# Kernel tuning notes

Measured on AMD Instinct MI355X. Metric: run time of the kernel, lower is better.

Reference implementation:

```python
import jax, jax.numpy as jnp
import numpy as np

B, S, ENC, DEC, ATTN, H = 256, 512, 256, 256, 128, 48

def setup_inputs() -> dict:
    key = jax.random.key(0)
    ks = jax.random.split(key, 12)
    n = jax.random.normal
    return {
        'enc_outputs': n(ks[0], (B, S, ENC), jnp.float32),
        'h0': n(ks[1], (B, DEC), jnp.float32),
        'c0': n(ks[2], (B, DEC), jnp.float32),
        'W_enc': n(ks[3], (ENC, ATTN), jnp.float32) * 0.05,
        'W_dec': n(ks[4], (DEC, ATTN), jnp.float32) * 0.05,
        'v': n(ks[5], (ATTN,), jnp.float32) * 0.05,
        'W_ih': n(ks[6], (4 * DEC, 1 + ENC), jnp.float32) * 0.05,
        'W_hh': n(ks[7], (4 * DEC, DEC), jnp.float32) * 0.05,
        'b_ih': n(ks[8], (4 * DEC,), jnp.float32) * 0.05,
        'b_hh': n(ks[9], (4 * DEC,), jnp.float32) * 0.05,
        'W_out': n(ks[10], (DEC,), jnp.float32) * 0.05,
        'b_out': n(ks[11], (1,), jnp.float32) * 0.05,
    }

def reference(enc_outputs, h0, c0, W_enc, W_dec, v, W_ih, W_hh, b_ih, b_hh, W_out, b_out):
    # Precompute encoder projection (constant across timesteps; same math as per-step).
    enc_proj = jnp.einsum('bse,ea->bsa', enc_outputs, W_enc)  # [B,S,ATTN]
    batch = enc_outputs.shape[0]
    inp0 = jnp.zeros((batch, 1), enc_outputs.dtype)

    def step(carry, _):
        h, c, inp = carry
        dec_proj = h @ W_dec  # [B,ATTN]
        scores = jnp.tanh(enc_proj + dec_proj[:, None, :]) @ v  # [B,S]
        attn_w = jax.nn.softmax(scores, axis=-1)
        context = jnp.einsum('bs,bse->be', attn_w, enc_outputs)  # [B,ENC]
        rnn_in = jnp.concatenate([inp, context], axis=-1)  # [B,1+ENC]
        gates = rnn_in @ W_ih.T + b_ih + h @ W_hh.T + b_hh  # [B,4*DEC]
        i, f, g, o = jnp.split(gates, 4, axis=-1)  # PyTorch LSTMCell gate order
        c_new = jax.nn.sigmoid(f) * c + jax.nn.sigmoid(i) * jnp.tanh(g)
        h_new = jax.nn.sigmoid(o) * jnp.tanh(c_new)
        out = h_new @ W_out + b_out[0]  # [B]
        return (h_new, c_new, out[:, None]), (out, attn_w)

    _, (preds, attn_seq) = jax.lax.scan(step, (h0, c0, inp0), None, length=H)
    preds = jnp.transpose(preds, (1, 0))        # [B,H]
    attn_seq = jnp.transpose(attn_seq, (1, 0, 2))  # [B,H,S]
    return preds, attn_seq
```

## Files before the change

kernel.cpp:

```cpp
#include <hip/hip_runtime.h>
#include <stdint.h>

#define LOG2E 1.4426950408889634f
#define SCOPE __HIP_MEMORY_SCOPE_AGENT

typedef short v8s __attribute__((ext_vector_type(8)));
typedef float v4f __attribute__((ext_vector_type(4)));

__device__ __forceinline__ uint32_t bf16r(float x){
  uint32_t u = __float_as_uint(x);
  return (u + 0x7fffu + ((u >> 16) & 1u)) >> 16;
}
__device__ __forceinline__ uint32_t pack2(float lo, float hi){
  return bf16r(lo) | (bf16r(hi) << 16);
}
__device__ __forceinline__ float unlo(uint32_t u){ return __uint_as_float(u << 16); }
__device__ __forceinline__ float unhi(uint32_t u){ return __uint_as_float(u & 0xffff0000u); }

__device__ __forceinline__ float fexp2(float x){ return __builtin_amdgcn_exp2f(x); }
__device__ __forceinline__ float frcp(float x){ return __builtin_amdgcn_rcpf(x); }
__device__ __forceinline__ float ftanh(float x){
  float e = fexp2(x * (2.0f * LOG2E));
  return 1.0f - 2.0f * frcp(e + 1.0f);
}
__device__ __forceinline__ float fsig(float x){
  return frcp(1.0f + fexp2(-x * LOG2E));
}
__device__ __forceinline__ float wave_sum(float x){
  #pragma unroll
  for(int o = 32; o; o >>= 1) x += __shfl_xor(x, o, 64);
  return x;
}

__device__ __forceinline__ unsigned flag_ld(const unsigned* p){
  return __hip_atomic_load(p, __ATOMIC_RELAXED, SCOPE);
}
__device__ __forceinline__ void flag_st(unsigned* p, unsigned v){
  __hip_atomic_store(p, v, __ATOMIC_RELAXED, SCOPE);
}
__device__ __forceinline__ float ldf_c(const float* p){
  return __hip_atomic_load(p, __ATOMIC_RELAXED, SCOPE);
}
__device__ __forceinline__ void stf_c(float* p, float v){
  __hip_atomic_store(p, v, __ATOMIC_RELAXED, SCOPE);
}
__device__ __forceinline__ uint64_t ld64_c(const uint64_t* p){
  return __hip_atomic_load(p, __ATOMIC_RELAXED, SCOPE);
}
__device__ __forceinline__ void st64_c(uint64_t* p, uint64_t v){
  __hip_atomic_store(p, v, __ATOMIC_RELAXED, SCOPE);
}
__device__ __forceinline__ void st16_c(unsigned short* p, unsigned short v){
  __hip_atomic_store(p, v, __ATOMIC_RELAXED, SCOPE);
}

__device__ __forceinline__ int gate_row(int jg){
  return (jg & 3) * 256 + (jg >> 6) * 16 + ((jg >> 2) & 15);
}

__global__ __launch_bounds__(256) void k_pack(const float* __restrict__ W_ih,
                                              const float* __restrict__ W_hh,
                                              const float* __restrict__ b_ih,
                                              const float* __restrict__ b_hh,
                                              const float* __restrict__ W_enc,
                                              unsigned short* __restrict__ WmT,
                                              float* __restrict__ biasc,
                                              float* __restrict__ w0v,
                                              unsigned short* __restrict__ WencTh,
                                              unsigned short* __restrict__ WencTl){
  int gid = blockIdx.x * 256 + threadIdx.x;
  if(gid < 65536){
    int jg = gid >> 6, k8 = gid & 63;
    int row = gate_row(jg);
    int k0 = k8 * 8;
    uint32_t p[4];
    #pragma unroll
    for(int mm = 0; mm < 4; ++mm){
      int ka = k0 + 2 * mm, kb = ka + 1;
      float lo = (ka < 256) ? W_ih[row * 257 + 1 + ka] : W_hh[row * 256 + (ka - 256)];
      float hi = (kb < 256) ? W_ih[row * 257 + 1 + kb] : W_hh[row * 256 + (kb - 256)];
      p[mm] = pack2(lo, hi);
    }
    *(uint4*)&WmT[(size_t)jg * 512 + k0] = make_uint4(p[0], p[1], p[2], p[3]);
    if(k8 == 0){
      biasc[jg] = b_ih[row] + b_hh[row];
      w0v[jg] = W_ih[row * 257];
    }
  } else {
    int g2 = gid - 65536;
    int k = g2 >> 7, a = g2 & 127;
    float x = W_enc[k * 128 + a];
    uint32_t hb = bf16r(x);
    WencTh[a * 256 + k] = (unsigned short)hb;
    float hv = __uint_as_float(hb << 16);
    WencTl[a * 256 + k] = (unsigned short)bf16r(x - hv);
  }
}

__global__ __launch_bounds__(256, 2) void k_enc_proj(const float* __restrict__ enc,
                                                     const unsigned short* __restrict__ WencTh,
                                                     const unsigned short* __restrict__ WencTl,
                                                     unsigned short* __restrict__ ep,
                                                     unsigned short* __restrict__ encbT){
  __shared__ unsigned short Ash[128][48];
  __shared__ unsigned short Asl[128][48];
  __shared__ unsigned short Wth[128][48];
  __shared__ unsigned short Wtl[128][48];
  const int tid = threadIdx.x;
  const int b = blockIdx.x >> 2, mt = blockIdx.x & 3;
  const int lane = tid & 63, w = tid >> 6;
  const int rr = lane & 15, quad = lane >> 4;

  v4f acc[2][8];
  #pragma unroll
  for(int g = 0; g < 2; ++g)
    #pragma unroll
    for(int nt = 0; nt < 8; ++nt) acc[g][nt] = (v4f){0.f, 0.f, 0.f, 0.f};

  const float* encBase = enc + ((size_t)(b * 512 + mt * 128)) * 256;

  for(int kt = 0; kt < 8; ++kt){
    __syncthreads();
    #pragma unroll
    for(int i = 0; i < 4; ++i){
      int flat = i * 256 + tid;
      int row = flat >> 3, c4 = flat & 7;
      float4 f = *(const float4*)(encBase + (size_t)row * 256 + kt * 32 + c4 * 4);
      uint32_t hx = bf16r(f.x), hy = bf16r(f.y), hz = bf16r(f.z), hw = bf16r(f.w);
      uint2 hp = make_uint2(hx | (hy << 16), hz | (hw << 16));
      float lx = f.x - __uint_as_float(hx << 16);
      float ly = f.y - __uint_as_float(hy << 16);
      float lz = f.z - __uint_as_float(hz << 16);
      float lw = f.w - __uint_as_float(hw << 16);
      uint2 lp = make_uint2(pack2(lx, ly), pack2(lz, lw));
      *(uint2*)&Ash[row][c4 * 4] = hp;
      *(uint2*)&Asl[row][c4 * 4] = lp;
    }
    #pragma unroll
    for(int i = 0; i < 2; ++i){
      int flat = i * 256 + tid;
      int a = flat >> 2, q4 = flat & 3;
      *(uint4*)&Wth[a][q4 * 8] = *(const uint4*)(WencTh + (size_t)a * 256 + kt * 32 + q4 * 8);
      *(uint4*)&Wtl[a][q4 * 8] = *(const uint4*)(WencTl + (size_t)a * 256 + kt * 32 + q4 * 8);
    }
    __syncthreads();
    #pragma unroll
    for(int g = 0; g < 2; ++g){
      v8s ah = *(const v8s*)&Ash[32 * w + 16 * g + rr][quad * 8];
      v8s al = *(const v8s*)&Asl[32 * w + 16 * g + rr][quad * 8];
      #pragma unroll
      for(int nt = 0; nt < 8; ++nt){
        v8s bh = *(const v8s*)&Wth[nt * 16 + rr][quad * 8];
        v8s bl = *(const v8s*)&Wtl[nt * 16 + rr][quad * 8];
        acc[g][nt] = __builtin_amdgcn_mfma_f32_16x16x32_bf16(ah, bh, acc[g][nt], 0, 0, 0);
        acc[g][nt] = __builtin_amdgcn_mfma_f32_16x16x32_bf16(al, bh, acc[g][nt], 0, 0, 0);
        acc[g][nt] = __builtin_amdgcn_mfma_f32_16x16x32_bf16(ah, bl, acc[g][nt], 0, 0, 0);
      }
    }
    {
      unsigned short* ebT = encbT + ((size_t)(b * 256 + kt * 32)) * 512 + mt * 128;
      #pragma unroll
      for(int i2 = 0; i2 < 2; ++i2){
        int flat = i2 * 256 + tid;
        int e_loc = flat & 31, sc = flat >> 5;
        unsigned short tmp[8];
        #pragma unroll
        for(int i = 0; i < 8; ++i) tmp[i] = Ash[sc * 8 + i][e_loc];
        *(uint4*)&ebT[(size_t)e_loc * 512 + sc * 8] = *(uint4*)tmp;
      }
    }
  }
  #pragma unroll
  for(int g = 0; g < 2; ++g){
    int s0 = 128 * mt + 32 * w + 16 * g + quad * 4;
    #pragma unroll
    for(int nt = 0; nt < 8; ++nt){
      int a = nt * 16 + rr;
      uint2 pp = make_uint2(pack2(acc[g][nt][0], acc[g][nt][1]),
                            pack2(acc[g][nt][2], acc[g][nt][3]));
      *(uint2*)&ep[((size_t)b * 128 + a) * 512 + s0] = pp;
    }
  }
}

__global__ __launch_bounds__(512) void k_zero(unsigned* __restrict__ fl){
  fl[threadIdx.x] = 0u;
}

__global__ __launch_bounds__(512, 2) void k_steps(
    const unsigned short* __restrict__ encbT, const unsigned short* __restrict__ ep,
    const unsigned short* __restrict__ WmT, const float* __restrict__ biasc,
    const float* __restrict__ w0v, const float* __restrict__ Wdec,
    const float* __restrict__ Wout, const float* __restrict__ h0,
    const float* __restrict__ c0, const float* __restrict__ v,
    const float* __restrict__ b_out, unsigned* __restrict__ flagA,
    unsigned* __restrict__ flagB, float* __restrict__ predf,
    float* __restrict__ dpp, float* __restrict__ predp,
    unsigned short* __restrict__ xcat2, float* __restrict__ out)
{
  __shared__ __align__(16) unsigned short WT[64][520];
  __shared__ __align__(16) unsigned short AT[16][520];
  __shared__ float WdecL[16][128];
  __shared__ float gact[64][20];
  __shared__ float dpf[128];
  __shared__ float vl[128];
  __shared__ float scp[64][65];
  __shared__ float red2[8];
  __shared__ float hf[256];
  __shared__ float dppart[4][128];
  __shared__ __align__(16) unsigned short abfh[512];
  __shared__ __align__(16) unsigned short abfl[512];
  __shared__ float biasL[64], w0L[64], WoutL[16], predfL[16];
  __shared__ float sB;

  const int tid = threadIdx.x, b = blockIdx.x;
  const int lane = tid & 63, wid = tid >> 6;
  const int quad = lane >> 4, rr = lane & 15;
  const int m16 = (b >> 4) << 4;
  const int n = b & 15;

  {
    const uint4* src = (const uint4*)(WmT + (size_t)(n * 64) * 512);
    #pragma unroll
    for(int i = 0; i < 8; ++i){
      int flat = i * 512 + tid;
      int r = flat >> 6, q = flat & 63;
      *(uint4*)&WT[r][q * 8] = src[r * 64 + q];
    }
    const float4* wsrc = (const float4*)(Wdec + (size_t)(n * 16) * 128);
    int r2 = tid >> 5, q2 = tid & 31;
    *(float4*)&WdecL[r2][q2 * 4] = wsrc[r2 * 32 + q2];
    if(tid < 64){ biasL[tid] = biasc[n * 64 + tid]; w0L[tid] = w0v[n * 64 + tid]; }
    if(tid < 16) WoutL[tid] = Wout[n * 16 + tid];
    if(tid < 128) vl[tid] = v[tid];
    if(tid == 0){ sB = b_out[0]; stf_c(&predf[b], 0.f); }
    #pragma unroll
    for(int i = 0; i < 8; ++i){
      int flat = i * 512 + tid;
      int r = flat >> 8, c = flat & 255;
      AT[r][256 + c] = (unsigned short)bf16r(h0[(size_t)(m16 + r) * 256 + c]);
    }
  }
  float c_reg = 0.f;
  if(tid < 256){
    int bl = tid >> 4, dl = tid & 15;
    c_reg = c0[(size_t)(m16 + bl) * 256 + n * 16 + dl];
    hf[tid] = h0[(size_t)b * 256 + tid];
  }
  __syncthreads();
  {
    int a = tid & 127, p = tid >> 7;
    float s = 0.f;
    const float* wd = Wdec + (size_t)(p * 64) * 128 + a;
    #pragma unroll 8
    for(int d = 0; d < 64; ++d) s += hf[p * 64 + d] * wd[(size_t)d * 128];
    dppart[p][a] = s;
  }
  __syncthreads();
  if(tid < 128) dpf[tid] = dppart[0][tid] + dppart[1][tid] + dppart[2][tid] + dppart[3][tid];
  __syncthreads();

  const uint4* ep4 = (const uint4*)(ep + (size_t)b * 65536);

  #pragma unroll 1
  for(int t = 0; t < 48; ++t){
    unsigned short* xcatP = xcat2 + (size_t)(t & 1) * 131072;
    unsigned short* xcatN = xcat2 + (size_t)((t + 1) & 1) * 131072;

    if(t > 0){
      if(tid < 16){
        unsigned want = (unsigned)t;
        while(flag_ld(&flagB[m16 + tid]) < want) __builtin_amdgcn_s_sleep(1);
      }
      __syncthreads();
      {
        const uint64_t* hsrc = (const uint64_t*)(xcatP + (size_t)m16 * 512);
        #pragma unroll
        for(int i = 0; i < 2; ++i){
          int flat = i * 512 + tid;
          int r = flat >> 6, q = flat & 63;
          *(uint64_t*)&AT[r][256 + q * 4] = ld64_c(hsrc + (size_t)r * 128 + 64 + q);
        }
      }
      if(tid < 128){
        float s = 0.f;
        #pragma unroll
        for(int nn = 0; nn < 16; ++nn) s += ldf_c(&dpp[((size_t)b * 16 + nn) * 128 + tid]);
        dpf[tid] = s;
      } else if(tid == 128){
        float pf = 0.f;
        #pragma unroll
        for(int nn = 0; nn < 16; ++nn) pf += ldf_c(&predp[nn * 256 + b]);
        pf += sB;
        out[b * 48 + (t - 1)] = pf;
        stf_c(&predf[b], pf);
      }
      __syncthreads();
    }

    uint4 u[16];
    #pragma unroll
    for(int i = 0; i < 16; ++i) u[i] = ep4[(wid * 16 + i) * 64 + lane];

    v4f acc = {0.f, 0.f, 0.f, 0.f};
    if(tid < 256){
      const int jl = (tid >> 6) * 16 + rr;
      #pragma unroll
      for(int kt = 8; kt < 16; ++kt){
        int k0 = kt * 32 + quad * 8;
        v8s av = *(const v8s*)&AT[rr][k0];
        v8s bv = *(const v8s*)&WT[jl][k0];
        acc = __builtin_amdgcn_mfma_f32_16x16x32_bf16(av, bv, acc, 0, 0, 0);
      }
    }

    {
      float sc[8];
      #pragma unroll
      for(int j = 0; j < 8; ++j) sc[j] = 0.f;
      #pragma unroll
      for(int i = 0; i < 16; ++i){
        int a = wid * 16 + i;
        float dd = dpf[a], vv = vl[a];
        sc[0] += vv * ftanh(unlo(u[i].x) + dd);
        sc[1] += vv * ftanh(unhi(u[i].x) + dd);
        sc[2] += vv * ftanh(unlo(u[i].y) + dd);
        sc[3] += vv * ftanh(unhi(u[i].y) + dd);
        sc[4] += vv * ftanh(unlo(u[i].z) + dd);
        sc[5] += vv * ftanh(unhi(u[i].z) + dd);
        sc[6] += vv * ftanh(unlo(u[i].w) + dd);
        sc[7] += vv * ftanh(unhi(u[i].w) + dd);
      }
      #pragma unroll
      for(int j = 0; j < 8; ++j) scp[j * 8 + wid][lane] = sc[j];
    }
    __syncthreads();

    float wexp;
    {
      float s = 0.f;
      #pragma unroll
      for(int q = 0; q < 8; ++q) s += scp[(tid & 7) * 8 + q][tid >> 3];
      wexp = fexp2(s * LOG2E);
      float sw = wave_sum(wexp);
      if(lane == 0) red2[wid] = sw;
    }
    __syncthreads();
    {
      float L = red2[0];
      #pragma unroll
      for(int i = 1; i < 8; ++i) L += red2[i];
      float aw = wexp * frcp(L);
      uint32_t ah = bf16r(aw);
      abfh[tid] = (unsigned short)ah;
      abfl[tid] = (unsigned short)bf16r(aw - __uint_as_float(ah << 16));
      out[12288 + (size_t)b * 24576 + t * 512 + tid] = aw;
    }
    __syncthreads();

    {
      const unsigned short* eT =
          encbT + ((size_t)(b * 256) + wid * 32 + rr) * 512 + quad * 8;
      v4f ca = {0.f, 0.f, 0.f, 0.f}, cb = {0.f, 0.f, 0.f, 0.f};
      #pragma unroll 4
      for(int kt = 0; kt < 16; ++kt){
        int k0 = kt * 32;
        v8s avh = *(const v8s*)&abfh[k0 + quad * 8];
        v8s avl = *(const v8s*)&abfl[k0 + quad * 8];
        v8s bv0 = *(const v8s*)(eT + k0);
        v8s bv1 = *(const v8s*)(eT + 16 * 512 + k0);
        ca = __builtin_amdgcn_mfma_f32_16x16x32_bf16(avh, bv0, ca, 0, 0, 0);
        ca = __builtin_amdgcn_mfma_f32_16x16x32_bf16(avl, bv0, ca, 0, 0, 0);
        cb = __builtin_amdgcn_mfma_f32_16x16x32_bf16(avh, bv1, cb, 0, 0, 0);
        cb = __builtin_amdgcn_mfma_f32_16x16x32_bf16(avl, bv1, cb, 0, 0, 0);
      }
      if(quad == 0){
        st16_c(&xcatP[(size_t)b * 512 + wid * 32 + rr], (unsigned short)bf16r(ca[0]));
        st16_c(&xcatP[(size_t)b * 512 + wid * 32 + 16 + rr], (unsigned short)bf16r(cb[0]));
      }
    }
    __syncthreads();
    if(tid == 0) flag_st(&flagA[b], (unsigned)(t + 1));

    if(tid < 16){
      unsigned want = (unsigned)(t + 1);
      while(flag_ld(&flagA[m16 + tid]) < want) __builtin_amdgcn_s_sleep(1);
    }
    __syncthreads();
    {
      const uint64_t* csrc = (const uint64_t*)(xcatP + (size_t)m16 * 512);
      #pragma unroll
      for(int i = 0; i < 2; ++i){
        int flat = i * 512 + tid;
        int r = flat >> 6, q = flat & 63;
        *(uint64_t*)&AT[r][q * 4] = ld64_c(csrc + (size_t)r * 128 + q);
      }
      if(tid < 16) predfL[tid] = ldf_c(&predf[m16 + tid]);
    }
    __syncthreads();
    if(tid < 256){
      const int jl = (tid >> 6) * 16 + rr;
      #pragma unroll
      for(int kt = 0; kt < 8; ++kt){
        int k0 = kt * 32 + quad * 8;
        v8s av = *(const v8s*)&AT[rr][k0];
        v8s bv = *(const v8s*)&WT[jl][k0];
        acc = __builtin_amdgcn_mfma_f32_16x16x32_bf16(av, bv, acc, 0, 0, 0);
      }
      float bias = biasL[jl], w0 = w0L[jl];
      int gate = jl & 3;
      #pragma unroll
      for(int r = 0; r < 4; ++r){
        int bl = quad * 4 + r;
        float pre = acc[r] + bias + predfL[bl] * w0;
        gact[jl][bl] = (gate == 2) ? ftanh(pre) : fsig(pre);
      }
    }
    __syncthreads();
    if(tid < 256){
      int bl = tid >> 4, dl = tid & 15;
      float gi = gact[dl * 4 + 0][bl];
      float gf = gact[dl * 4 + 1][bl];
      float gg = gact[dl * 4 + 2][bl];
      float go = gact[dl * 4 + 3][bl];
      int bg = m16 + bl, dg = n * 16 + dl;
      float cn = gf * c_reg + gi * gg;
      c_reg = cn;
      float hn = go * ftanh(cn);
      st16_c(&xcatN[(size_t)bg * 512 + 256 + dg], (unsigned short)bf16r(hn));
      float pp = hn * WoutL[dl];
      #pragma unroll
      for(int o = 8; o; o >>= 1) pp += __shfl_xor(pp, o, 64);
      if(dl == 0) stf_c(&predp[n * 256 + bg], pp);
      float a0[8] = {0, 0, 0, 0, 0, 0, 0, 0};
      #pragma unroll
      for(int d = 0; d < 16; ++d){
        float hv = __shfl(hn, (lane & 48) + d, 64);
        #pragma unroll
        for(int j = 0; j < 8; ++j) a0[j] += hv * WdecL[d][dl * 8 + j];
      }
      float* dst = &dpp[((size_t)bg * 16 + n) * 128 + dl * 8];
      #pragma unroll
      for(int j = 0; j < 4; ++j){
        uint64_t uu = (uint64_t)__float_as_uint(a0[2 * j]) |
                      ((uint64_t)__float_as_uint(a0[2 * j + 1]) << 32);
        st64_c((uint64_t*)(dst + 2 * j), uu);
      }
    }
    __syncthreads();
    if(tid == 0) flag_st(&flagB[b], (unsigned)(t + 1));
  }

  if(tid < 16){
    while(flag_ld(&flagB[m16 + tid]) < 48u) __builtin_amdgcn_s_sleep(1);
  }
  __syncthreads();
  if(tid == 0){
    float pf = 0.f;
    #pragma unroll
    for(int nn = 0; nn < 16; ++nn) pf += ldf_c(&predp[nn * 256 + b]);
    out[b * 48 + 47] = pf + sB;
  }
}

extern "C" void kernel_launch(void* const* d_in, const int* in_sizes, int n_in,
                              void* d_out, int out_size, void* d_ws, size_t ws_size,
                              hipStream_t stream) {
  (void)in_sizes; (void)n_in; (void)out_size; (void)ws_size;
  const float* enc  = (const float*)d_in[0];
  const float* h0   = (const float*)d_in[1];
  const float* c0   = (const float*)d_in[2];
  const float* Wenc = (const float*)d_in[3];
  const float* Wdec = (const float*)d_in[4];
  const float* v    = (const float*)d_in[5];
  const float* Wih  = (const float*)d_in[6];
  const float* Whh  = (const float*)d_in[7];
  const float* bih  = (const float*)d_in[8];
  const float* bhh  = (const float*)d_in[9];
  const float* Wout = (const float*)d_in[10];
  const float* bout = (const float*)d_in[11];
  float* out = (float*)d_out;
  uint8_t* p = (uint8_t*)d_ws;

  unsigned short* encbT = (unsigned short*)p; p += 67108864ull;
  unsigned short* ep = (unsigned short*)p;  p += 33554432ull;
  unsigned short* WmT = (unsigned short*)p; p += 1048576ull;
  float* biasc  = (float*)p;                p += 4096ull;
  float* w0v    = (float*)p;                p += 4096ull;
  unsigned short* WencTh = (unsigned short*)p; p += 131072ull;
  unsigned short* WencTl = (unsigned short*)p; p += 131072ull;
  float* dpp    = (float*)p;                p += 2097152ull;
  float* predp  = (float*)p;                p += 16384ull;
  unsigned short* xcat2 = (unsigned short*)p; p += 524288ull;

  unsigned* flagA = (unsigned*)WencTh;
  unsigned* flagB = flagA + 256;
  float*    predf = (float*)(flagA + 512);

  k_pack<<<dim3(384), dim3(256), 0, stream>>>(Wih, Whh, bih, bhh, Wenc, WmT, biasc, w0v,
                                              WencTh, WencTl);
  k_enc_proj<<<dim3(1024), dim3(256), 0, stream>>>(enc, WencTh, WencTl, ep, encbT);
  k_zero<<<dim3(1), dim3(512), 0, stream>>>(flagA);
  k_steps<<<dim3(256), dim3(512), 0, stream>>>(encbT, ep, WmT, biasc, w0v, Wdec, Wout,
                                               h0, c0, v, bout, flagA, flagB, predf,
                                               dpp, predp, xcat2, out);
}
```

Measured before the change: 1.241 ms.

## Double step-kernel block size, restructure score loop and dec projection via MFMA

The persistent step kernel now runs 1024 threads per block instead of 512. The attention-score loop is reorganised so each thread handles one sequence position over half of the attention dimension, reading the encoder projection directly rather than staging it in registers. The per-step h@W_dec partial product moves from a scalar FMA loop to bf16 MFMA with a hi/lo split of h and W_dec. The context MFMA is split across more waves, the context is staged in LDS before a coalesced store, and predp is transposed for contiguous reads. The extra threads are meant to raise latency hiding and parallelism, at the cost of more registers and LDS pressure per block and some extra barriers.

```diff
diff --git a/kernel.cpp b/kernel.cpp
--- a/kernel.cpp
+++ b/kernel.cpp
@@ -187,7 +187,7 @@
   fl[threadIdx.x] = 0u;
 }
 
-__global__ __launch_bounds__(512, 2) void k_steps(
+__global__ __launch_bounds__(1024, 4) void k_steps(
     const unsigned short* __restrict__ encbT, const unsigned short* __restrict__ ep,
     const unsigned short* __restrict__ WmT, const float* __restrict__ biasc,
     const float* __restrict__ w0v, const float* __restrict__ Wdec,
@@ -195,21 +195,24 @@
     const float* __restrict__ c0, const float* __restrict__ v,
     const float* __restrict__ b_out, unsigned* __restrict__ flagA,
     unsigned* __restrict__ flagB, float* __restrict__ predf,
-    float* __restrict__ dpp, float* __restrict__ predp,
+    float* __restrict__ dpp, float* __restrict__ predpT,
     unsigned short* __restrict__ xcat2, float* __restrict__ out)
 {
   __shared__ __align__(16) unsigned short WT[64][520];
   __shared__ __align__(16) unsigned short AT[16][520];
-  __shared__ float WdecL[16][128];
+  __shared__ __align__(16) unsigned short WbB1[8][4][16][8];
+  __shared__ __align__(16) unsigned short WbB2[8][4][16][8];
+  __shared__ __align__(16) unsigned short hbfA[16 * 40];
   __shared__ float gact[64][20];
   __shared__ float dpf[128];
   __shared__ float vl[128];
-  __shared__ float scp[64][65];
+  __shared__ float scpS[2][512];
   __shared__ float red2[8];
   __shared__ float hf[256];
   __shared__ float dppart[4][128];
   __shared__ __align__(16) unsigned short abfh[512];
   __shared__ __align__(16) unsigned short abfl[512];
+  __shared__ __align__(16) unsigned short ctxb[256];
   __shared__ float biasL[64], w0L[64], WoutL[16], predfL[16];
   __shared__ float sB;
 
@@ -222,21 +225,32 @@
   {
     const uint4* src = (const uint4*)(WmT + (size_t)(n * 64) * 512);
     #pragma unroll
-    for(int i = 0; i < 8; ++i){
-      int flat = i * 512 + tid;
+    for(int i = 0; i < 4; ++i){
+      int flat = i * 1024 + tid;
       int r = flat >> 6, q = flat & 63;
       *(uint4*)&WT[r][q * 8] = src[r * 64 + q];
     }
-    const float4* wsrc = (const float4*)(Wdec + (size_t)(n * 16) * 128);
-    int r2 = tid >> 5, q2 = tid & 31;
-    *(float4*)&WdecL[r2][q2 * 4] = wsrc[r2 * 32 + q2];
+    #pragma unroll
+    for(int i = 0; i < 2; ++i){
+      int flat = i * 1024 + tid;
+      int d = flat >> 7, a = flat & 127;
+      float wv = Wdec[(size_t)(n * 16 + d) * 128 + a];
+      uint32_t hb = bf16r(wv);
+      float hv = __uint_as_float(hb << 16);
+      uint32_t lb = bf16r(wv - hv);
+      int ac = a >> 4, cr = a & 15, qd = d >> 3, ii = d & 7;
+      WbB1[ac][qd][cr][ii] = (unsigned short)hb;
+      WbB1[ac][2 + qd][cr][ii] = (unsigned short)hb;
+      WbB2[ac][qd][cr][ii] = (unsigned short)lb;
+      WbB2[ac][2 + qd][cr][ii] = 0;
+    }
     if(tid < 64){ biasL[tid] = biasc[n * 64 + tid]; w0L[tid] = w0v[n * 64 + tid]; }
     if(tid < 16) WoutL[tid] = Wout[n * 16 + tid];
     if(tid < 128) vl[tid] = v[tid];
     if(tid == 0){ sB = b_out[0]; stf_c(&predf[b], 0.f); }
     #pragma unroll
-    for(int i = 0; i < 8; ++i){
-      int flat = i * 512 + tid;
+    for(int i = 0; i < 4; ++i){
+      int flat = i * 1024 + tid;
       int r = flat >> 8, c = flat & 255;
       AT[r][256 + c] = (unsigned short)bf16r(h0[(size_t)(m16 + r) * 256 + c]);
     }
@@ -248,7 +262,7 @@
     hf[tid] = h0[(size_t)b * 256 + tid];
   }
   __syncthreads();
-  {
+  if(tid < 512){
     int a = tid & 127, p = tid >> 7;
     float s = 0.f;
     const float* wd = Wdec + (size_t)(p * 64) * 128 + a;
@@ -260,8 +274,6 @@
   if(tid < 128) dpf[tid] = dppart[0][tid] + dppart[1][tid] + dppart[2][tid] + dppart[3][tid];
   __syncthreads();
 
-  const uint4* ep4 = (const uint4*)(ep + (size_t)b * 65536);
-
   #pragma unroll 1
   for(int t = 0; t < 48; ++t){
     unsigned short* xcatP = xcat2 + (size_t)(t & 1) * 131072;
@@ -275,12 +287,8 @@
       __syncthreads();
       {
         const uint64_t* hsrc = (const uint64_t*)(xcatP + (size_t)m16 * 512);
-        #pragma unroll
-        for(int i = 0; i < 2; ++i){
-          int flat = i * 512 + tid;
-          int r = flat >> 6, q = flat & 63;
-          *(uint64_t*)&AT[r][256 + q * 4] = ld64_c(hsrc + (size_t)r * 128 + 64 + q);
-        }
+        int r = tid >> 6, q = tid & 63;
+        *(uint64_t*)&AT[r][256 + q * 4] = ld64_c(hsrc + (size_t)r * 128 + 64 + q);
       }
       if(tid < 128){
         float s = 0.f;
@@ -290,17 +298,13 @@
       } else if(tid == 128){
         float pf = 0.f;
         #pragma unroll
-        for(int nn = 0; nn < 16; ++nn) pf += ldf_c(&predp[nn * 256 + b]);
+        for(int nn = 0; nn < 16; ++nn) pf += ldf_c(&predpT[b * 16 + nn]);
         pf += sB;
         out[b * 48 + (t - 1)] = pf;
         stf_c(&predf[b], pf);
       }
       __syncthreads();
     }
-
-    uint4 u[16];
-    #pragma unroll
-    for(int i = 0; i < 16; ++i) u[i] = ep4[(wid * 16 + i) * 64 + lane];
 
     v4f acc = {0.f, 0.f, 0.f, 0.f};
     if(tid < 256){
@@ -315,72 +319,62 @@
     }
 
     {
-      float sc[8];
-      #pragma unroll
-      for(int j = 0; j < 8; ++j) sc[j] = 0.f;
-      #pragma unroll
-      for(int i = 0; i < 16; ++i){
-        int a = wid * 16 + i;
-        float dd = dpf[a], vv = vl[a];
-        sc[0] += vv * ftanh(unlo(u[i].x) + dd);
-        sc[1] += vv * ftanh(unhi(u[i].x) + dd);
-        sc[2] += vv * ftanh(unlo(u[i].y) + dd);
-        sc[3] += vv * ftanh(unhi(u[i].y) + dd);
-        sc[4] += vv * ftanh(unlo(u[i].z) + dd);
-        sc[5] += vv * ftanh(unhi(u[i].z) + dd);
-        sc[6] += vv * ftanh(unlo(u[i].w) + dd);
-        sc[7] += vv * ftanh(unhi(u[i].w) + dd);
-      }
-      #pragma unroll
-      for(int j = 0; j < 8; ++j) scp[j * 8 + wid][lane] = sc[j];
-    }
-    __syncthreads();
-
-    float wexp;
+      int s = tid & 511, ah = tid >> 9;
+      const unsigned short* eps = ep + (size_t)b * 65536 + (size_t)(ah * 64) * 512 + s;
+      float sc = 0.f;
+      #pragma unroll 8
+      for(int a = 0; a < 64; ++a){
+        float ev = __uint_as_float((uint32_t)eps[(size_t)a * 512] << 16);
+        int ag = ah * 64 + a;
+        sc += vl[ag] * ftanh(ev + dpf[ag]);
+      }
+      scpS[ah][s] = sc;
+    }
+    __syncthreads();
+
+    float aw = 0.f;
     {
-      float s = 0.f;
-      #pragma unroll
-      for(int q = 0; q < 8; ++q) s += scp[(tid & 7) * 8 + q][tid >> 3];
-      wexp = fexp2(s * LOG2E);
-      float sw = wave_sum(wexp);
-      if(lane == 0) red2[wid] = sw;
-    }
-    __syncthreads();
-    {
-      float L = red2[0];
-      #pragma unroll
-      for(int i = 1; i < 8; ++i) L += red2[i];
-      float aw = wexp * frcp(L);
-      uint32_t ah = bf16r(aw);
-      abfh[tid] = (unsigned short)ah;
-      abfl[tid] = (unsigned short)bf16r(aw - __uint_as_float(ah << 16));
-      out[12288 + (size_t)b * 24576 + t * 512 + tid] = aw;
+      float wexp = 0.f;
+      if(tid < 512){
+        float s = scpS[0][tid] + scpS[1][tid];
+        wexp = fexp2(s * LOG2E);
+        float sw = wave_sum(wexp);
+        if(lane == 0) red2[wid] = sw;
+      }
+      __syncthreads();
+      if(tid < 512){
+        float L = red2[0];
+        #pragma unroll
+        for(int i = 1; i < 8; ++i) L += red2[i];
+        aw = wexp * frcp(L);
+        uint32_t ah2 = bf16r(aw);
+        abfh[tid] = (unsigned short)ah2;
+        abfl[tid] = (unsigned short)bf16r(aw - __uint_as_float(ah2 << 16));
+      }
     }
     __syncthreads();
 
     {
       const unsigned short* eT =
-          encbT + ((size_t)(b * 256) + wid * 32 + rr) * 512 + quad * 8;
-      v4f ca = {0.f, 0.f, 0.f, 0.f}, cb = {0.f, 0.f, 0.f, 0.f};
-      #pragma unroll 4
+          encbT + ((size_t)(b * 256) + wid * 16 + rr) * 512 + quad * 8;
+      v4f ca = {0.f, 0.f, 0.f, 0.f};
+      #pragma unroll 8
       for(int kt = 0; kt < 16; ++kt){
         int k0 = kt * 32;
         v8s avh = *(const v8s*)&abfh[k0 + quad * 8];
         v8s avl = *(const v8s*)&abfl[k0 + quad * 8];
-        v8s bv0 = *(const v8s*)(eT + k0);
-        v8s bv1 = *(const v8s*)(eT + 16 * 512 + k0);
-        ca = __builtin_amdgcn_mfma_f32_16x16x32_bf16(avh, bv0, ca, 0, 0, 0);
-        ca = __builtin_amdgcn_mfma_f32_16x16x32_bf16(avl, bv0, ca, 0, 0, 0);
-        cb = __builtin_amdgcn_mfma_f32_16x16x32_bf16(avh, bv1, cb, 0, 0, 0);
-        cb = __builtin_amdgcn_mfma_f32_16x16x32_bf16(avl, bv1, cb, 0, 0, 0);
-      }
-      if(quad == 0){
-        st16_c(&xcatP[(size_t)b * 512 + wid * 32 + rr], (unsigned short)bf16r(ca[0]));
-        st16_c(&xcatP[(size_t)b * 512 + wid * 32 + 16 + rr], (unsigned short)bf16r(cb[0]));
-      }
-    }
+        v8s bv = *(const v8s*)(eT + k0);
+        ca = __builtin_amdgcn_mfma_f32_16x16x32_bf16(avh, bv, ca, 0, 0, 0);
+        ca = __builtin_amdgcn_mfma_f32_16x16x32_bf16(avl, bv, ca, 0, 0, 0);
+      }
+      if(quad == 0) ctxb[wid * 16 + rr] = (unsigned short)bf16r(ca[0]);
+    }
+    __syncthreads();
+    if(tid < 64)
+      st64_c((uint64_t*)(xcatP + (size_t)b * 512) + tid, ((const uint64_t*)ctxb)[tid]);
     __syncthreads();
     if(tid == 0) flag_st(&flagA[b], (unsigned)(t + 1));
+    if(tid < 512) out[12288 + (size_t)b * 24576 + t * 512 + tid] = aw;
 
     if(tid < 16){
       unsigned want = (unsigned)(t + 1);
@@ -389,12 +383,8 @@
     __syncthreads();
     {
       const uint64_t* csrc = (const uint64_t*)(xcatP + (size_t)m16 * 512);
-      #pragma unroll
-      for(int i = 0; i < 2; ++i){
-        int flat = i * 512 + tid;
-        int r = flat >> 6, q = flat & 63;
-        *(uint64_t*)&AT[r][q * 4] = ld64_c(csrc + (size_t)r * 128 + q);
-      }
+      int r = tid >> 6, q = tid & 63;
+      *(uint64_t*)&AT[r][q * 4] = ld64_c(csrc + (size_t)r * 128 + q);
       if(tid < 16) predfL[tid] = ldf_c(&predf[m16 + tid]);
     }
     __syncthreads();
@@ -427,24 +417,27 @@
       float cn = gf * c_reg + gi * gg;
       c_reg = cn;
       float hn = go * ftanh(cn);
-      st16_c(&xcatN[(size_t)bg * 512 + 256 + dg], (unsigned short)bf16r(hn));
+      uint32_t hh = bf16r(hn);
+      st16_c(&xcatN[(size_t)bg * 512 + 256 + dg], (unsigned short)hh);
+      hbfA[bl * 40 + dl] = (unsigned short)hh;
+      hbfA[bl * 40 + 16 + dl] = (unsigned short)bf16r(hn - __uint_as_float(hh << 16));
       float pp = hn * WoutL[dl];
       #pragma unroll
       for(int o = 8; o; o >>= 1) pp += __shfl_xor(pp, o, 64);
-      if(dl == 0) stf_c(&predp[n * 256 + bg], pp);
-      float a0[8] = {0, 0, 0, 0, 0, 0, 0, 0};
-      #pragma unroll
-      for(int d = 0; d < 16; ++d){
-        float hv = __shfl(hn, (lane & 48) + d, 64);
-        #pragma unroll
-        for(int j = 0; j < 8; ++j) a0[j] += hv * WdecL[d][dl * 8 + j];
-      }
-      float* dst = &dpp[((size_t)bg * 16 + n) * 128 + dl * 8];
-      #pragma unroll
-      for(int j = 0; j < 4; ++j){
-        uint64_t uu = (uint64_t)__float_as_uint(a0[2 * j]) |
-                      ((uint64_t)__float_as_uint(a0[2 * j + 1]) << 32);
-        st64_c((uint64_t*)(dst + 2 * j), uu);
+      if(dl == 0) stf_c(&predpT[bg * 16 + n], pp);
+    }
+    __syncthreads();
+    if(tid < 512){
+      v8s av = *(const v8s*)&hbfA[rr * 40 + quad * 8];
+      v8s b1 = *(const v8s*)&WbB1[wid][quad][rr][0];
+      v8s b2 = *(const v8s*)&WbB2[wid][quad][rr][0];
+      v4f dacc = {0.f, 0.f, 0.f, 0.f};
+      dacc = __builtin_amdgcn_mfma_f32_16x16x32_bf16(av, b1, dacc, 0, 0, 0);
+      dacc = __builtin_amdgcn_mfma_f32_16x16x32_bf16(av, b2, dacc, 0, 0, 0);
+      #pragma unroll
+      for(int r = 0; r < 4; ++r){
+        int bl = quad * 4 + r;
+        stf_c(&dpp[((size_t)(m16 + bl) * 16 + n) * 128 + wid * 16 + rr], dacc[r]);
       }
     }
     __syncthreads();
@@ -458,7 +451,7 @@
   if(tid == 0){
     float pf = 0.f;
     #pragma unroll
-    for(int nn = 0; nn < 16; ++nn) pf += ldf_c(&predp[nn * 256 + b]);
+    for(int nn = 0; nn < 16; ++nn) pf += ldf_c(&predpT[b * 16 + nn]);
     out[b * 48 + 47] = pf + sB;
   }
 }
@@ -490,7 +483,7 @@
   unsigned short* WencTh = (unsigned short*)p; p += 131072ull;
   unsigned short* WencTl = (unsigned short*)p; p += 131072ull;
   float* dpp    = (float*)p;                p += 2097152ull;
-  float* predp  = (float*)p;                p += 16384ull;
+  float* predpT = (float*)p;                p += 16384ull;
   unsigned short* xcat2 = (unsigned short*)p; p += 524288ull;
 
   unsigned* flagA = (unsigned*)WencTh;
@@ -501,7 +494,7 @@
                                               WencTh, WencTl);
   k_enc_proj<<<dim3(1024), dim3(256), 0, stream>>>(enc, WencTh, WencTl, ep, encbT);
   k_zero<<<dim3(1), dim3(512), 0, stream>>>(flagA);
-  k_steps<<<dim3(256), dim3(512), 0, stream>>>(encbT, ep, WmT, biasc, w0v, Wdec, Wout,
-                                               h0, c0, v, bout, flagA, flagB, predf,
-                                               dpp, predp, xcat2, out);
-}
+  k_steps<<<dim3(256), dim3(1024), 0, stream>>>(encbT, ep, WmT, biasc, w0v, Wdec, Wout,
+                                                h0, c0, v, bout, flagA, flagB, predf,
+                                                dpp, predpT, xcat2, out);
+}
```

Result: no change. 1.253 ms (+1.0%).
